# Kernel tuning notes

Measured on AMD Instinct MI355X. Metric: run time of the kernel, lower is better.

The kernel has to match this reference:

```python
import jax, jax.numpy as jnp
import numpy as np

CTX = 2048
D_IN = 2048
D_OUT = 2048
N_HEADS = 16
HEAD_DIM = D_OUT // N_HEADS
ROPE_BASE = 10000.0


def rope_tables(head_dim, ctx):
    inv_freq = 1.0 / (ROPE_BASE ** (jnp.arange(0, head_dim, 2, dtype=jnp.float32) / head_dim))
    angles = jnp.arange(ctx, dtype=jnp.float32)[:, None] * inv_freq[None, :]  # [ctx, hd/2]
    angles = jnp.concatenate([angles, angles], axis=1)  # [ctx, hd]
    return jnp.sin(angles), jnp.cos(angles)


def apply_rope(x, sin, cos):
    # x: [b, h, s, d]; rotate-by-half (Raschka / Llama style)
    s = x.shape[2]
    d = x.shape[3]
    x1, x2 = x[..., : d // 2], x[..., d // 2 :]
    rotated = jnp.concatenate([-x2, x1], axis=-1)
    return x * cos[:s][None, None] + rotated * sin[:s][None, None]


def setup_inputs() -> dict:
    key = jax.random.key(0)
    kx, kq, kk, kv, ko = jax.random.split(key, 5)
    scale = 0.02
    return {
        "x": jax.random.normal(kx, (2, CTX, D_IN), dtype=jnp.float32),
        "W_query": jax.random.normal(kq, (D_IN, D_OUT), dtype=jnp.float32) * scale,
        "W_key": jax.random.normal(kk, (D_IN, D_OUT), dtype=jnp.float32) * scale,
        "W_value": jax.random.normal(kv, (D_IN, D_OUT), dtype=jnp.float32) * scale,
        "W_out": jax.random.normal(ko, (D_OUT, D_OUT), dtype=jnp.float32) * scale,
    }


def reference(x, W_query, W_key, W_value, W_out):
    bs, cl, _ = x.shape
    sin, cos = rope_tables(HEAD_DIM, CTX)

    def split_heads(t):  # [b, s, d_out] -> [b, h, s, hd]
        return t.reshape(bs, cl, N_HEADS, HEAD_DIM).transpose(0, 2, 1, 3)

    q = split_heads(x @ W_query)
    k = split_heads(x @ W_key)
    v = split_heads(x @ W_value)

    q = apply_rope(q, sin, cos)
    k = apply_rope(k, sin, cos)

    # NOTE: original module does NOT scale by 1/sqrt(head_dim)
    scores = jnp.einsum("bhqd,bhkd->bhqk", q, k)
    causal = jnp.triu(jnp.ones((cl, cl), dtype=bool), k=1)
    scores = jnp.where(causal[None, None], -jnp.inf, scores)
    weights = jax.nn.softmax(scores, axis=-1)
    ctx = jnp.einsum("bhqk,bhkd->bhqd", weights, v)
    ctx = ctx.transpose(0, 2, 1, 3).reshape(bs, cl, N_HEADS * HEAD_DIM)
    return ctx @ W_out
```

## Files before the change

### kernel.cpp

```cpp
#include <hip/hip_runtime.h>
#include <cstdint>
#include <cstddef>

typedef _Float16 f16;
typedef _Float16 f16x8 __attribute__((ext_vector_type(8)));
typedef _Float16 f16x4 __attribute__((ext_vector_type(4)));
typedef float    f32x4 __attribute__((ext_vector_type(4)));

#define S_CTX 2048
#define NH 16
#define DH 128

#define BAR() asm volatile("s_barrier" ::: "memory")
#define VMW(n) asm volatile("s_waitcnt vmcnt(" #n ")" ::: "memory")

__device__ __forceinline__ void gload16(const void* g, void* l) {
  __builtin_amdgcn_global_load_lds(
      (const __attribute__((address_space(1))) void*)g,
      (__attribute__((address_space(3))) void*)l, 16, 0, 0);
}

__global__ void prep(const float* __restrict__ x,
                     const float* __restrict__ w0, const float* __restrict__ w1,
                     const float* __restrict__ w2, const float* __restrict__ w3,
                     f16* __restrict__ xb,
                     f16* __restrict__ o0, f16* __restrict__ o1,
                     f16* __restrict__ o2, f16* __restrict__ o3,
                     float* __restrict__ sint, float* __restrict__ cost) {
  const int bid = blockIdx.x, tid = threadIdx.x;
  if (bid < 512) {
    int idx = bid * 256 + tid;
    int j = idx & 63, s = idx >> 6;
    float invf = __expf(-(float)(2 * j) * (1.0f / 128.0f) * 9.210340371976184f);
    float a = (float)s * invf;
    sint[idx] = sinf(a);
    cost[idx] = cosf(a);
  } else if (bid < 8704) {
    int i = ((bid - 512) * 256 + tid) * 4;
    float4 v = *(const float4*)(x + i);
    f16x4 o; o[0] = (f16)v.x; o[1] = (f16)v.y; o[2] = (f16)v.z; o[3] = (f16)v.w;
    *(f16x4*)(xb + i) = o;
  } else {
    int b2 = bid - 8704;
    int z = b2 >> 12, rem = b2 & 4095;
    int by = rem >> 6, bx = rem & 63;
    int tx = tid & 31, ty = tid >> 5;
    const float* in; f16* out;
    switch (z) {
      case 0: in = w0; out = o0; break;
      case 1: in = w1; out = o1; break;
      case 2: in = w2; out = o2; break;
      default: in = w3; out = o3; break;
    }
    __shared__ float tl[32][33];
    int xc = bx * 32 + tx, yc = by * 32 + ty;
#pragma unroll
    for (int r = 0; r < 32; r += 8)
      tl[ty + r][tx] = in[(size_t)(yc + r) * 2048 + xc];
    __syncthreads();
    int xo = by * 32 + tx, yo = bx * 32 + ty;
#pragma unroll
    for (int r = 0; r < 32; r += 8)
      out[(size_t)(yo + r) * 2048 + xo] = (f16)tl[tx][ty + r];
  }
}

template<bool OUTP>
__global__ __launch_bounds__(512, 1)
void gemm8(const f16* __restrict__ A,
           const f16* __restrict__ wq, const f16* __restrict__ wk, const f16* __restrict__ wv,
           f16* __restrict__ qb, f16* __restrict__ kb, f16* __restrict__ vtb,
           float* __restrict__ of,
           const float* __restrict__ sint, const float* __restrict__ cost) {
  extern __shared__ __align__(16) char lds[];
#define RING_A(e) (lds + (e) * 16384)
#define RING_B(e) (lds + 65536 + (e) * 8192)
  const int tid = threadIdx.x, lane = tid & 63;
  const int wvi = tid >> 6, wm = wvi >> 1, wn = wvi & 1;
  const int gcol = blockIdx.x * 128;
  const int proj = OUTP ? 0 : (gcol >> 11);
  const int col0 = OUTP ? gcol : (gcol & 2047);
  const int row0 = blockIdx.y * 256;
  const f16* Bt = OUTP ? wq : (proj == 0 ? wq : (proj == 1 ? wk : wv));

  const int ca0 = tid, ca1 = tid + 512, cb0 = tid;
  const int rAs0 = ca0 >> 2, rAs1 = ca1 >> 2, rBs0 = cb0 >> 2;
  const int sA0 = (ca0 & 3) ^ ((rAs0 >> 1) & 3);
  const int sA1 = (ca1 & 3) ^ ((rAs1 >> 1) & 3);
  const int sB0 = (cb0 & 3) ^ ((rBs0 >> 1) & 3);
  const f16* gA0 = A + (size_t)(row0 + rAs0) * 2048 + sA0 * 8;
  const f16* gA1 = A + (size_t)(row0 + rAs1) * 2048 + sA1 * 8;
  const f16* gB0 = Bt + (size_t)(col0 + rBs0) * 2048 + sB0 * 8;

  const int kslot = lane >> 4;
  int aoff[4], boff[4];
#pragma unroll
  for (int i = 0; i < 4; i++) {
    int row = wm * 64 + i * 16 + (lane & 15);
    aoff[i] = row * 64 + ((kslot ^ ((row >> 1) & 3)) << 4);
  }
#pragma unroll
  for (int j = 0; j < 4; j++) {
    int rb = wn * 32 + (j & 1) * 16 + (j >> 1) * 64 + (lane & 15);
    boff[j] = rb * 64 + ((kslot ^ ((rb >> 1) & 3)) << 4);
  }

  f32x4 acc[4][4] = {};

#define PHASE(SLOT, HS, DOSTAGE, WN) do {                                      \
    const char* As_ = RING_A(SLOT);                                            \
    const char* Bs_ = RING_B(SLOT);                                            \
    f16x8 af[4], bf[4];                                                        \
    _Pragma("unroll") for (int i_ = 0; i_ < 4; i_++)                           \
      af[i_] = *(const f16x8*)(As_ + aoff[i_]);                                \
    _Pragma("unroll") for (int j_ = 0; j_ < 4; j_++)                           \
      bf[j_] = *(const f16x8*)(Bs_ + boff[j_]);                                \
    if (DOSTAGE) {                                                             \
      gload16(gA0 + (HS) * 32, RING_A((HS) & 3) + ca0 * 16);                   \
      gload16(gA1 + (HS) * 32, RING_A((HS) & 3) + ca1 * 16);                   \
      gload16(gB0 + (HS) * 32, RING_B((HS) & 3) + cb0 * 16);                   \
    }                                                                          \
    asm volatile("s_waitcnt vmcnt(" #WN ")" ::: "memory");                     \
    BAR();                                                                     \
    __builtin_amdgcn_s_setprio(1);                                             \
    _Pragma("unroll") for (int i_ = 0; i_ < 4; i_++)                           \
      _Pragma("unroll") for (int j_ = 0; j_ < 4; j_++)                         \
        acc[i_][j_] = __builtin_amdgcn_mfma_f32_16x16x32_f16(af[i_], bf[j_],   \
                                                             acc[i_][j_], 0, 0, 0); \
    __builtin_amdgcn_s_setprio(0);                                             \
    BAR();                                                                     \
  } while (0)

#pragma unroll
  for (int h = 0; h < 3; h++) {
    gload16(gA0 + h * 32, RING_A(h) + ca0 * 16);
    gload16(gA1 + h * 32, RING_A(h) + ca1 * 16);
    gload16(gB0 + h * 32, RING_B(h) + cb0 * 16);
  }
  VMW(6); BAR();

  for (int t = 0; t < 15; ++t) {
    const int p = t * 4;
    PHASE(0, p + 3, 1, 6);
    PHASE(1, p + 4, 1, 6);
    PHASE(2, p + 5, 1, 6);
    PHASE(3, p + 6, 1, 6);
  }
  PHASE(0, 63, 1, 6);
  PHASE(1, 0, 0, 3);
  PHASE(2, 0, 0, 0);
  PHASE(3, 0, 0, 63);
#undef PHASE

  const int b = row0 >> 11, sbase = row0 & 2047;

  if (OUTP) {
#pragma unroll
    for (int i = 0; i < 4; i++)
#pragma unroll
      for (int j = 0; j < 4; j++)
#pragma unroll
        for (int r = 0; r < 4; r++) {
          int row = row0 + wm * 64 + i * 16 + (lane >> 4) * 4 + r;
          int col = col0 + wn * 32 + (j & 1) * 16 + (j >> 1) * 64 + (lane & 15);
          of[(size_t)row * 2048 + col] = acc[i][j][r];
        }
  } else if (proj < 2) {
    f16* dst = proj ? kb : qb;
    const int h = col0 >> 7;
#pragma unroll
    for (int i = 0; i < 4; i++)
#pragma unroll
      for (int jj = 0; jj < 2; jj++)
#pragma unroll
        for (int r = 0; r < 4; r++) {
          int s = sbase + wm * 64 + i * 16 + (lane >> 4) * 4 + r;
          int d = wn * 32 + jj * 16 + (lane & 15);
          float cv = cost[s * 64 + d], sv = sint[s * 64 + d];
          float x1 = acc[i][jj][r], x2 = acc[i][jj + 2][r];
          size_t base = ((size_t)(b * NH + h) * S_CTX + s) << 7;
          dst[base + d]      = (f16)(x1 * cv - x2 * sv);
          dst[base + d + 64] = (f16)(x2 * cv + x1 * sv);
        }
  } else {
    const int h = col0 >> 7;
    f16x4* ldsv = (f16x4*)lds;
#pragma unroll
    for (int i = 0; i < 4; i++)
#pragma unroll
      for (int j = 0; j < 4; j++) {
        f16x4 v;
#pragma unroll
        for (int r = 0; r < 4; r++) v[r] = (f16)acc[i][j][r];
        int su = wm * 16 + i * 4 + (lane >> 4);
        int d  = wn * 32 + (j & 1) * 16 + (j >> 1) * 64 + (lane & 15);
        ldsv[d * 64 + (su ^ ((d << 1) & 63))] = v;
      }
    __syncthreads();
#pragma unroll
    for (int it = 0; it < 8; ++it) {
      int o = it * 512 + tid;
      int d = o >> 5, c = o & 31;
      int xc = (d << 1) & 63;
      f16x4 lo = ldsv[d * 64 + ((2 * c) ^ xc)];
      f16x4 hi = ldsv[d * 64 + ((2 * c + 1) ^ xc)];
      f16x8 vv;
      vv[0] = lo[0]; vv[1] = lo[1]; vv[2] = lo[2]; vv[3] = lo[3];
      vv[4] = hi[0]; vv[5] = hi[1]; vv[6] = hi[2]; vv[7] = hi[3];
      *(f16x8*)&vtb[((size_t)(b * NH + h) * DH + d) * S_CTX + sbase + c * 8] = vv;
    }
  }
#undef RING_A
#undef RING_B
}

__global__ __launch_bounds__(256)
void attn_k(const f16* __restrict__ q, const f16* __restrict__ kk,
            const f16* __restrict__ vt, f16* __restrict__ ctx) {
  __shared__ __align__(16) f16 Ks[64 * 128];
  __shared__ __align__(16) f16 Vs[128 * 64];
  __shared__ __align__(16) f16 Pl[4][16 * 64];
  const int tid = threadIdx.x, lane = tid & 63, wv = tid >> 6;
  const int bh = blockIdx.y;
  const int b = bh >> 4, h = bh & 15;
  const size_t plane = (size_t)bh * (S_CTX * DH);
  const f16* Qp = q + plane;
  const f16* Kp = kk + plane;
  const f16* Vp = vt + plane;
  const float LOG2E = 1.4426950408889634f;

  for (int half = 0; half < 2; half++) {
    const int qt = half ? (31 - (int)blockIdx.x) : (int)blockIdx.x;
    const int q0 = qt * 64;

    f16x8 qf[4];
    {
      const f16* qq = Qp + (size_t)(q0 + wv * 16 + (lane & 15)) * DH + ((lane >> 4) * 8);
#pragma unroll
      for (int ks = 0; ks < 4; ks++) {
        qf[ks] = *(const f16x8*)(qq + ks * 32);
#pragma unroll
        for (int e = 0; e < 8; e++) qf[ks][e] = (f16)((float)qf[ks][e] * LOG2E);
      }
    }
    float m_[4], l_[4];
    f32x4 o[8] = {};
#pragma unroll
    for (int r = 0; r < 4; r++) { m_[r] = -3e38f; l_[r] = 0.f; }

    for (int t = 0; t <= qt; t++) {
      __syncthreads();
#pragma unroll
      for (int j = 0; j < 4; j++) {
        int c = tid + j * 256;
        int row = c >> 4, sl = (c & 15) ^ (row & 7);
        gload16(Kp + (size_t)(t * 64 + row) * DH + sl * 8, Ks + c * 8);
      }
#pragma unroll
      for (int j = 0; j < 4; j++) {
        int c = tid + j * 256;
        int row = c >> 3, sl = (c & 7) ^ (row & 7);
        gload16(Vp + (size_t)row * S_CTX + t * 64 + sl * 8, Vs + c * 8);
      }
      __syncthreads();

      f32x4 st[4] = {};
#pragma unroll
      for (int n = 0; n < 4; n++) {
        int rK = n * 16 + (lane & 15);
#pragma unroll
        for (int ks = 0; ks < 4; ks++) {
          int slot = ks * 4 + (lane >> 4);
          f16x8 kf = *(const f16x8*)&Ks[rK * 128 + ((slot ^ (rK & 7)) << 3)];
          st[n] = __builtin_amdgcn_mfma_f32_16x16x32_f16(qf[ks], kf, st[n], 0, 0, 0);
        }
      }
      if (t == qt) {
#pragma unroll
        for (int n = 0; n < 4; n++)
#pragma unroll
          for (int r = 0; r < 4; r++) {
            int kvc = n * 16 + (lane & 15);
            int qr = wv * 16 + (lane >> 4) * 4 + r;
            if (kvc > qr) st[n][r] = -3e38f;
          }
      }
      float mx[4];
#pragma unroll
      for (int r = 0; r < 4; r++)
        mx[r] = fmaxf(fmaxf(st[0][r], st[1][r]), fmaxf(st[2][r], st[3][r]));
#pragma unroll
      for (int msk = 1; msk < 16; msk <<= 1)
#pragma unroll
        for (int r = 0; r < 4; r++) mx[r] = fmaxf(mx[r], __shfl_xor(mx[r], msk));
      bool need = false;
#pragma unroll
      for (int r = 0; r < 4; r++) need = need || (mx[r] > m_[r] + 8.0f);
      if (__any(need)) {
#pragma unroll
        for (int r = 0; r < 4; r++) {
          float nm = fmaxf(m_[r], mx[r]);
          float al = __builtin_amdgcn_exp2f(m_[r] - nm);
          m_[r] = nm;
          l_[r] *= al;
#pragma unroll
          for (int j = 0; j < 8; j++) o[j][r] *= al;
        }
      }
      float ps[4] = {0.f, 0.f, 0.f, 0.f};
      float pvv[4][4];
#pragma unroll
      for (int n = 0; n < 4; n++)
#pragma unroll
        for (int r = 0; r < 4; r++) {
          float p = __builtin_amdgcn_exp2f(st[n][r] - m_[r]);
          pvv[n][r] = p; ps[r] += p;
        }
#pragma unroll
      for (int msk = 1; msk < 16; msk <<= 1)
#pragma unroll
        for (int r = 0; r < 4; r++) ps[r] += __shfl_xor(ps[r], msk);
#pragma unroll
      for (int r = 0; r < 4; r++) l_[r] += ps[r];

      f16* Pw = Pl[wv];
#pragma unroll
      for (int n = 0; n < 4; n++)
#pragma unroll
        for (int r = 0; r < 4; r++) {
          int rowp = (lane >> 4) * 4 + r;
          int colp = n * 16 + (lane & 15);
          Pw[rowp * 64 + (((colp >> 3) ^ (rowp & 7)) << 3) + (colp & 7)] = (f16)pvv[n][r];
        }
#pragma unroll
      for (int ks = 0; ks < 2; ks++) {
        int rowp = lane & 15;
        int slotp = ks * 4 + (lane >> 4);
        f16x8 pa = *(const f16x8*)&Pw[rowp * 64 + ((slotp ^ (rowp & 7)) << 3)];
#pragma unroll
        for (int j = 0; j < 8; j++) {
          int rv = j * 16 + (lane & 15);
          int slotv = ks * 4 + (lane >> 4);
          f16x8 vf = *(const f16x8*)&Vs[rv * 64 + ((slotv ^ (rv & 7)) << 3)];
          o[j] = __builtin_amdgcn_mfma_f32_16x16x32_f16(pa, vf, o[j], 0, 0, 0);
        }
      }
    }

#pragma unroll
    for (int j = 0; j < 8; j++)
#pragma unroll
      for (int r = 0; r < 4; r++) {
        int qr = q0 + wv * 16 + (lane >> 4) * 4 + r;
        int dd = h * 128 + j * 16 + (lane & 15);
        ctx[((size_t)(b * S_CTX + qr) * 2048) + dd] = (f16)(o[j][r] / l_[r]);
      }
  }
}

extern "C" void kernel_launch(void* const* d_in, const int* in_sizes, int n_in,
                              void* d_out, int out_size, void* d_ws, size_t ws_size,
                              hipStream_t stream) {
  (void)in_sizes; (void)n_in; (void)out_size; (void)ws_size;
  const float* x  = (const float*)d_in[0];
  const float* Wq = (const float*)d_in[1];
  const float* Wk = (const float*)d_in[2];
  const float* Wv = (const float*)d_in[3];
  const float* Wo = (const float*)d_in[4];
  float* out = (float*)d_out;
  char* ws = (char*)d_ws;

  f16*   xb   = (f16*)(ws);
  f16*   ctxb = (f16*)(ws);
  f16*   wqT  = (f16*)(ws + 16777216);
  f16*   wkT  = (f16*)(ws + 25165824);
  f16*   wvT  = (f16*)(ws + 33554432);
  f16*   woT  = (f16*)(ws + 41943040);
  f16*   qb   = (f16*)(ws + 50331648);
  f16*   kb   = (f16*)(ws + 67108864);
  f16*   vtb  = (f16*)(ws + 83886080);
  float* sint = (float*)(ws + 100663296);
  float* cost = (float*)(ws + 101187584);

  prep<<<dim3(25088), dim3(256), 0, stream>>>(x, Wq, Wk, Wv, Wo, xb,
                                              wqT, wkT, wvT, woT, sint, cost);
  gemm8<false><<<dim3(48, 16), dim3(512), 98304, stream>>>(
      xb, wqT, wkT, wvT, qb, kb, vtb, nullptr, sint, cost);
  attn_k<<<dim3(16, 32), dim3(256), 0, stream>>>(qb, kb, vtb, ctxb);
  gemm8<true><<<dim3(16, 16), dim3(512), 98304, stream>>>(
      ctxb, woT, woT, woT, nullptr, nullptr, nullptr, out, nullptr, nullptr);
}
```

Before: 280.8 us.

## Split QKV GEMM into 256x256 QK kernel and V kernel; double-buffer attention

The fused QKV projection is split in two. A new gemm_qk kernel uses 256x256 tiles with a 3-slot LDS ring and applies RoPE in its epilogue, and the V projection gets its own gemm8 launch. The attention kernel moves to 512 threads, with 128-row query tiles per block and double-buffered K/V tiles in LDS, so loads of the next tile overlap compute on the current one. The aim is more data reuse per tile and less load latency in attention. The cost is larger register and LDS footprints, one extra kernel launch, and fewer attention blocks (256), which may limit occupancy.

```diff
diff --git a/kernel.cpp b/kernel.cpp
--- a/kernel.cpp
+++ b/kernel.cpp
@@ -65,23 +65,122 @@
   }
 }
 
-template<bool OUTP>
 __global__ __launch_bounds__(512, 1)
-void gemm8(const f16* __restrict__ A,
-           const f16* __restrict__ wq, const f16* __restrict__ wk, const f16* __restrict__ wv,
-           f16* __restrict__ qb, f16* __restrict__ kb, f16* __restrict__ vtb,
-           float* __restrict__ of,
-           const float* __restrict__ sint, const float* __restrict__ cost) {
+void gemm_qk(const f16* __restrict__ A, const f16* __restrict__ wqT,
+             const f16* __restrict__ wkT,
+             f16* __restrict__ qb, f16* __restrict__ kb,
+             const float* __restrict__ sint, const float* __restrict__ cost) {
+  extern __shared__ __align__(16) char lds[];
+  const int tid = threadIdx.x, lane = tid & 63;
+  const int wvi = tid >> 6, wm = wvi >> 2, wn = wvi & 3;
+  const int gcol = blockIdx.x * 256;
+  const int proj = gcol >> 11;
+  const int col0 = gcol & 2047;
+  const int row0 = blockIdx.y * 256;
+  const f16* Bt = proj ? wkT : wqT;
+
+  const int ca0 = tid, ca1 = tid + 512;
+  const int ra0 = ca0 >> 2, ra1 = ca1 >> 2;
+  const int sa0 = (ca0 & 3) ^ ((ra0 >> 1) & 3);
+  const int sa1 = (ca1 & 3) ^ ((ra1 >> 1) & 3);
+  const f16* gA0 = A + (size_t)(row0 + ra0) * 2048 + sa0 * 8;
+  const f16* gA1 = A + (size_t)(row0 + ra1) * 2048 + sa1 * 8;
+  const f16* gB0 = Bt + (size_t)(col0 + ra0) * 2048 + sa0 * 8;
+  const f16* gB1 = Bt + (size_t)(col0 + ra1) * 2048 + sa1 * 8;
+
+  const int kslot = lane >> 4;
+  int aoff[8], boff[4];
+#pragma unroll
+  for (int i = 0; i < 8; i++) {
+    int row = wm * 128 + i * 16 + (lane & 15);
+    aoff[i] = row * 64 + ((kslot ^ ((row >> 1) & 3)) << 4);
+  }
+#pragma unroll
+  for (int j = 0; j < 4; j++) {
+    int rb = (wn >> 1) * 128 + (wn & 1) * 32 + (j & 1) * 16 + (j >> 1) * 64 + (lane & 15);
+    boff[j] = rb * 64 + ((kslot ^ ((rb >> 1) & 3)) << 4);
+  }
+
+  f32x4 acc[8][4] = {};
+
+#define QKPH(SLOT, HS, SSLOT, DOSTAGE, WN) do {                                \
+    const char* As_ = lds + (SLOT) * 32768;                                    \
+    const char* Bs_ = As_ + 16384;                                             \
+    f16x8 af[8], bf[4];                                                        \
+    _Pragma("unroll") for (int i_ = 0; i_ < 8; i_++)                           \
+      af[i_] = *(const f16x8*)(As_ + aoff[i_]);                                \
+    _Pragma("unroll") for (int j_ = 0; j_ < 4; j_++)                           \
+      bf[j_] = *(const f16x8*)(Bs_ + boff[j_]);                                \
+    if (DOSTAGE) {                                                             \
+      char* dA = lds + (SSLOT) * 32768;                                        \
+      gload16(gA0 + (HS) * 32, dA + ca0 * 16);                                 \
+      gload16(gA1 + (HS) * 32, dA + ca1 * 16);                                 \
+      gload16(gB0 + (HS) * 32, dA + 16384 + ca0 * 16);                         \
+      gload16(gB1 + (HS) * 32, dA + 16384 + ca1 * 16);                         \
+    }                                                                          \
+    asm volatile("s_waitcnt vmcnt(" #WN ")" ::: "memory");                     \
+    BAR();                                                                     \
+    __builtin_amdgcn_s_setprio(1);                                             \
+    _Pragma("unroll") for (int i_ = 0; i_ < 8; i_++)                           \
+      _Pragma("unroll") for (int j_ = 0; j_ < 4; j_++)                         \
+        acc[i_][j_] = __builtin_amdgcn_mfma_f32_16x16x32_f16(af[i_], bf[j_],   \
+                                                             acc[i_][j_], 0, 0, 0); \
+    __builtin_amdgcn_s_setprio(0);                                             \
+    BAR();                                                                     \
+  } while (0)
+
+#pragma unroll
+  for (int h = 0; h < 2; h++) {
+    char* dA = lds + h * 32768;
+    gload16(gA0 + h * 32, dA + ca0 * 16);
+    gload16(gA1 + h * 32, dA + ca1 * 16);
+    gload16(gB0 + h * 32, dA + 16384 + ca0 * 16);
+    gload16(gB1 + h * 32, dA + 16384 + ca1 * 16);
+  }
+  VMW(4); BAR();
+
+  for (int t = 0; t < 20; ++t) {
+    const int hb = 3 * t;
+    QKPH(0, hb + 2, 2, 1, 4);
+    QKPH(1, hb + 3, 0, 1, 4);
+    QKPH(2, hb + 4, 1, 1, 4);
+  }
+  QKPH(0, 62, 2, 1, 4);
+  QKPH(1, 63, 0, 1, 4);
+  QKPH(2, 0, 0, 0, 0);
+  QKPH(0, 0, 0, 0, 63);
+#undef QKPH
+
+  const int b = row0 >> 11, sb = row0 & 2047;
+  f16* dst = proj ? kb : qb;
+  const int h = (col0 >> 7) + (wn >> 1);
+#pragma unroll
+  for (int i = 0; i < 8; i++)
+#pragma unroll
+    for (int jj = 0; jj < 2; jj++)
+#pragma unroll
+      for (int r = 0; r < 4; r++) {
+        int s = sb + wm * 128 + i * 16 + (lane >> 4) * 4 + r;
+        int d = (wn & 1) * 32 + jj * 16 + (lane & 15);
+        float cv = cost[s * 64 + d], sv = sint[s * 64 + d];
+        float x1 = acc[i][jj][r], x2 = acc[i][jj + 2][r];
+        size_t base = ((size_t)(b * NH + h) * S_CTX + s) << 7;
+        dst[base + d]      = (f16)(x1 * cv - x2 * sv);
+        dst[base + d + 64] = (f16)(x2 * cv + x1 * sv);
+      }
+}
+
+template<int MODE>
+__global__ __launch_bounds__(512, 1)
+void gemm8(const f16* __restrict__ A, const f16* __restrict__ Bt,
+           f16* __restrict__ vtb, float* __restrict__ of) {
   extern __shared__ __align__(16) char lds[];
 #define RING_A(e) (lds + (e) * 16384)
 #define RING_B(e) (lds + 65536 + (e) * 8192)
   const int tid = threadIdx.x, lane = tid & 63;
   const int wvi = tid >> 6, wm = wvi >> 1, wn = wvi & 1;
-  const int gcol = blockIdx.x * 128;
-  const int proj = OUTP ? 0 : (gcol >> 11);
-  const int col0 = OUTP ? gcol : (gcol & 2047);
+  const int col0 = blockIdx.x * 128;
   const int row0 = blockIdx.y * 256;
-  const f16* Bt = OUTP ? wq : (proj == 0 ? wq : (proj == 1 ? wk : wv));
 
   const int ca0 = tid, ca1 = tid + 512, cb0 = tid;
   const int rAs0 = ca0 >> 2, rAs1 = ca1 >> 2, rBs0 = cb0 >> 2;
@@ -107,7 +206,7 @@
 
   f32x4 acc[4][4] = {};
 
-#define PHASE(SLOT, HS, DOSTAGE, WN) do {                                      \
+#define PH8(SLOT, HS, DOSTAGE, WN) do {                                        \
     const char* As_ = RING_A(SLOT);                                            \
     const char* Bs_ = RING_B(SLOT);                                            \
     f16x8 af[4], bf[4];                                                        \
@@ -141,20 +240,20 @@
 
   for (int t = 0; t < 15; ++t) {
     const int p = t * 4;
-    PHASE(0, p + 3, 1, 6);
-    PHASE(1, p + 4, 1, 6);
-    PHASE(2, p + 5, 1, 6);
-    PHASE(3, p + 6, 1, 6);
-  }
-  PHASE(0, 63, 1, 6);
-  PHASE(1, 0, 0, 3);
-  PHASE(2, 0, 0, 0);
-  PHASE(3, 0, 0, 63);
-#undef PHASE
+    PH8(0, p + 3, 1, 6);
+    PH8(1, p + 4, 1, 6);
+    PH8(2, p + 5, 1, 6);
+    PH8(3, p + 6, 1, 6);
+  }
+  PH8(0, 63, 1, 6);
+  PH8(1, 0, 0, 3);
+  PH8(2, 0, 0, 0);
+  PH8(3, 0, 0, 63);
+#undef PH8
 
   const int b = row0 >> 11, sbase = row0 & 2047;
 
-  if (OUTP) {
+  if (MODE == 2) {
 #pragma unroll
     for (int i = 0; i < 4; i++)
 #pragma unroll
@@ -164,23 +263,6 @@
           int row = row0 + wm * 64 + i * 16 + (lane >> 4) * 4 + r;
           int col = col0 + wn * 32 + (j & 1) * 16 + (j >> 1) * 64 + (lane & 15);
           of[(size_t)row * 2048 + col] = acc[i][j][r];
-        }
-  } else if (proj < 2) {
-    f16* dst = proj ? kb : qb;
-    const int h = col0 >> 7;
-#pragma unroll
-    for (int i = 0; i < 4; i++)
-#pragma unroll
-      for (int jj = 0; jj < 2; jj++)
-#pragma unroll
-        for (int r = 0; r < 4; r++) {
-          int s = sbase + wm * 64 + i * 16 + (lane >> 4) * 4 + r;
-          int d = wn * 32 + jj * 16 + (lane & 15);
-          float cv = cost[s * 64 + d], sv = sint[s * 64 + d];
-          float x1 = acc[i][jj][r], x2 = acc[i][jj + 2][r];
-          size_t base = ((size_t)(b * NH + h) * S_CTX + s) << 7;
-          dst[base + d]      = (f16)(x1 * cv - x2 * sv);
-          dst[base + d + 64] = (f16)(x2 * cv + x1 * sv);
         }
   } else {
     const int h = col0 >> 7;
@@ -214,12 +296,12 @@
 #undef RING_B
 }
 
-__global__ __launch_bounds__(256)
+__global__ __launch_bounds__(512)
 void attn_k(const f16* __restrict__ q, const f16* __restrict__ kk,
             const f16* __restrict__ vt, f16* __restrict__ ctx) {
-  __shared__ __align__(16) f16 Ks[64 * 128];
-  __shared__ __align__(16) f16 Vs[128 * 64];
-  __shared__ __align__(16) f16 Pl[4][16 * 64];
+  __shared__ __align__(16) f16 Ks[2][64 * 128];
+  __shared__ __align__(16) f16 Vs[2][128 * 64];
+  __shared__ __align__(16) f16 Pl[8][16 * 64];
   const int tid = threadIdx.x, lane = tid & 63, wv = tid >> 6;
   const int bh = blockIdx.y;
   const int b = bh >> 4, h = bh & 15;
@@ -229,9 +311,13 @@
   const f16* Vp = vt + plane;
   const float LOG2E = 1.4426950408889634f;
 
+  const int ck0 = tid, ck1 = tid + 512;
+  const int cv0 = tid, cv1 = tid + 512;
+
   for (int half = 0; half < 2; half++) {
-    const int qt = half ? (31 - (int)blockIdx.x) : (int)blockIdx.x;
-    const int q0 = qt * 64;
+    const int Q = half ? (15 - (int)blockIdx.x) : (int)blockIdx.x;
+    const int q0 = Q * 128;
+    const int NT = 2 * Q + 2;
 
     f16x8 qf[4];
     {
@@ -248,21 +334,32 @@
 #pragma unroll
     for (int r = 0; r < 4; r++) { m_[r] = -3e38f; l_[r] = 0.f; }
 
-    for (int t = 0; t <= qt; t++) {
-      __syncthreads();
-#pragma unroll
-      for (int j = 0; j < 4; j++) {
-        int c = tid + j * 256;
-        int row = c >> 4, sl = (c & 15) ^ (row & 7);
-        gload16(Kp + (size_t)(t * 64 + row) * DH + sl * 8, Ks + c * 8);
-      }
-#pragma unroll
-      for (int j = 0; j < 4; j++) {
-        int c = tid + j * 256;
-        int row = c >> 3, sl = (c & 7) ^ (row & 7);
-        gload16(Vp + (size_t)row * S_CTX + t * 64 + sl * 8, Vs + c * 8);
-      }
-      __syncthreads();
+    {
+      int rk0 = ck0 >> 4, rk1 = ck1 >> 4;
+      gload16(Kp + (size_t)rk0 * DH + (((ck0 & 15) ^ (rk0 & 7)) * 8), &Ks[0][ck0 * 8]);
+      gload16(Kp + (size_t)rk1 * DH + (((ck1 & 15) ^ (rk1 & 7)) * 8), &Ks[0][ck1 * 8]);
+      int rv0 = cv0 >> 3, rv1 = cv1 >> 3;
+      gload16(Vp + (size_t)rv0 * S_CTX + (((cv0 & 7) ^ (rv0 & 7)) * 8), &Vs[0][cv0 * 8]);
+      gload16(Vp + (size_t)rv1 * S_CTX + (((cv1 & 7) ^ (rv1 & 7)) * 8), &Vs[0][cv1 * 8]);
+    }
+    VMW(0); BAR();
+
+    int cur = 0;
+    for (int t = 0; t < NT; t++) {
+      if (t + 1 < NT) {
+        const f16* Kt = Kp + (size_t)(t + 1) * 64 * DH;
+        const f16* Vt = Vp + (size_t)(t + 1) * 64;
+        int nb = cur ^ 1;
+        int rk0 = ck0 >> 4, rk1 = ck1 >> 4;
+        gload16(Kt + (size_t)rk0 * DH + (((ck0 & 15) ^ (rk0 & 7)) * 8), &Ks[nb][ck0 * 8]);
+        gload16(Kt + (size_t)rk1 * DH + (((ck1 & 15) ^ (rk1 & 7)) * 8), &Ks[nb][ck1 * 8]);
+        int rv0 = cv0 >> 3, rv1 = cv1 >> 3;
+        gload16(Vt + (size_t)rv0 * S_CTX + (((cv0 & 7) ^ (rv0 & 7)) * 8), &Vs[nb][cv0 * 8]);
+        gload16(Vt + (size_t)rv1 * S_CTX + (((cv1 & 7) ^ (rv1 & 7)) * 8), &Vs[nb][cv1 * 8]);
+      }
+
+      const f16* Ksc = Ks[cur];
+      const f16* Vsc = Vs[cur];
 
       f32x4 st[4] = {};
 #pragma unroll
@@ -271,17 +368,17 @@
 #pragma unroll
         for (int ks = 0; ks < 4; ks++) {
           int slot = ks * 4 + (lane >> 4);
-          f16x8 kf = *(const f16x8*)&Ks[rK * 128 + ((slot ^ (rK & 7)) << 3)];
+          f16x8 kf = *(const f16x8*)&Ksc[rK * 128 + ((slot ^ (rK & 7)) << 3)];
           st[n] = __builtin_amdgcn_mfma_f32_16x16x32_f16(qf[ks], kf, st[n], 0, 0, 0);
         }
       }
-      if (t == qt) {
+      if (t >= 2 * Q) {
 #pragma unroll
         for (int n = 0; n < 4; n++)
 #pragma unroll
           for (int r = 0; r < 4; r++) {
-            int kvc = n * 16 + (lane & 15);
-            int qr = wv * 16 + (lane >> 4) * 4 + r;
+            int kvc = t * 64 + n * 16 + (lane & 15);
+            int qr = q0 + wv * 16 + (lane >> 4) * 4 + r;
             if (kvc > qr) st[n][r] = -3e38f;
           }
       }
@@ -341,10 +438,13 @@
         for (int j = 0; j < 8; j++) {
           int rv = j * 16 + (lane & 15);
           int slotv = ks * 4 + (lane >> 4);
-          f16x8 vf = *(const f16x8*)&Vs[rv * 64 + ((slotv ^ (rv & 7)) << 3)];
+          f16x8 vf = *(const f16x8*)&Vsc[rv * 64 + ((slotv ^ (rv & 7)) << 3)];
           o[j] = __builtin_amdgcn_mfma_f32_16x16x32_f16(pa, vf, o[j], 0, 0, 0);
         }
       }
+
+      VMW(0); BAR();
+      cur ^= 1;
     }
 
 #pragma unroll
@@ -384,9 +484,8 @@
 
   prep<<<dim3(25088), dim3(256), 0, stream>>>(x, Wq, Wk, Wv, Wo, xb,
                                               wqT, wkT, wvT, woT, sint, cost);
-  gemm8<false><<<dim3(48, 16), dim3(512), 98304, stream>>>(
-      xb, wqT, wkT, wvT, qb, kb, vtb, nullptr, sint, cost);
-  attn_k<<<dim3(16, 32), dim3(256), 0, stream>>>(qb, kb, vtb, ctxb);
-  gemm8<true><<<dim3(16, 16), dim3(512), 98304, stream>>>(
-      ctxb, woT, woT, woT, nullptr, nullptr, nullptr, out, nullptr, nullptr);
-}
+  gemm_qk<<<dim3(16, 16), dim3(512), 98304, stream>>>(xb, wqT, wkT, qb, kb, sint, cost);
+  gemm8<1><<<dim3(16, 16), dim3(512), 98304, stream>>>(xb, wvT, vtb, nullptr);
+  attn_k<<<dim3(8, 32), dim3(512), 0, stream>>>(qb, kb, vtb, ctxb);
+  gemm8<2><<<dim3(16, 16), dim3(512), 98304, stream>>>(ctxb, woT, nullptr, out);
+}
```

Measured after the change: 274.9 us. 1.02x faster.
